# Kernel tuning notes

Measured on AMD Instinct MI355X. Metric: run time of the kernel, lower is better.

## Reference

```python
import jax, jax.numpy as jnp
import numpy as np

# Model dims (MiniCPM-style decode-only LM inside VoxCPM2)
L, B, D = 16, 4, 1024
H, HD, KVH = 16, 64, 8          # query heads, head dim, KV heads (GQA)
DFF = 4096
S = 2048                         # current KV cache length
SCALE_DEPTH = 1.4                # mup depth scaling
EPS = 1e-5
THETA = 10000.0
W_STD = 0.02


def setup_inputs() -> dict:
    key = jax.random.key(0)
    ks = jax.random.split(key, 12)
    return {
        "inputs_embeds": jax.random.normal(ks[0], (B, D), jnp.float32),
        "k_cache": jax.random.normal(ks[1], (L, B, KVH, S, HD), jnp.float32),
        "v_cache": jax.random.normal(ks[2], (L, B, KVH, S, HD), jnp.float32),
        "ln1_w": jnp.ones((L, D), jnp.float32),
        "ln2_w": jnp.ones((L, D), jnp.float32),
        "norm_w": jnp.ones((D,), jnp.float32),
        "wq": jax.random.normal(ks[3], (L, D, H * HD), jnp.float32) * W_STD,
        "wk": jax.random.normal(ks[4], (L, D, KVH * HD), jnp.float32) * W_STD,
        "wv": jax.random.normal(ks[5], (L, D, KVH * HD), jnp.float32) * W_STD,
        "wo": jax.random.normal(ks[6], (L, H * HD, D), jnp.float32) * W_STD,
        "w_gate": jax.random.normal(ks[7], (L, D, DFF), jnp.float32) * W_STD,
        "w_up": jax.random.normal(ks[8], (L, D, DFF), jnp.float32) * W_STD,
        "w_down": jax.random.normal(ks[9], (L, DFF, D), jnp.float32) * W_STD,
        "cache_length": S,  # position id of the token being decoded
    }


def _rmsnorm(x, w):
    return x * jax.lax.rsqrt(jnp.mean(x * x, axis=-1, keepdims=True) + EPS) * w


def _rotate_half(x):
    x1, x2 = jnp.split(x, 2, axis=-1)
    return jnp.concatenate((-x2, x1), axis=-1)


def _decode_step(inputs_embeds, k_cache, v_cache, ln1_w, ln2_w, norm_w,
                 wq, wk, wv, wo, w_gate, w_up, w_down, cache_length):
    # RoPE tables for the single decode position
    pos = jnp.asarray(cache_length, jnp.float32)
    inv_freq = 1.0 / (THETA ** (jnp.arange(0, HD, 2, dtype=jnp.float32) / HD))
    freqs = pos * inv_freq                       # [HD/2]
    emb = jnp.concatenate((freqs, freqs))        # [HD]
    cos, sin = jnp.cos(emb), jnp.sin(emb)

    mup = SCALE_DEPTH / np.sqrt(L)
    scale = 1.0 / np.sqrt(HD)
    G = H // KVH  # query heads per KV head

    def layer(h, ws):
        l1, l2, Wq, Wk, Wv, Wo, Wg, Wu, Wd, kc, vc = ws
        x = _rmsnorm(h, l1)                                  # [B, D]
        q = (x @ Wq).reshape(B, H, HD)
        k = (x @ Wk).reshape(B, KVH, HD)
        v = (x @ Wv).reshape(B, KVH, HD)
        q = q * cos + _rotate_half(q) * sin
        k = k * cos + _rotate_half(k) * sin
        nk = jnp.concatenate((kc, k[:, :, None, :]), axis=2)  # [B, KVH, S+1, HD]
        nv = jnp.concatenate((vc, v[:, :, None, :]), axis=2)
        qg = q.reshape(B, KVH, G, HD)                         # GQA grouping
        scores = jnp.einsum('bkgd,bksd->bkgs', qg, nk) * scale
        p = jax.nn.softmax(scores, axis=-1)
        o = jnp.einsum('bkgs,bksd->bkgd', p, nv).reshape(B, H * HD)
        h = h + (o @ Wo) * mup                                # mup residual
        x = _rmsnorm(h, l2)
        mlp = (jax.nn.silu(x @ Wg) * (x @ Wu)) @ Wd           # SwiGLU
        h = h + mlp * mup
        return h, (nk, nv)

    h, (next_k, next_v) = jax.lax.scan(
        layer, inputs_embeds,
        (ln1_w, ln2_w, wq, wk, wv, wo, w_gate, w_up, w_down, k_cache, v_cache))
    h = _rmsnorm(h, norm_w)
    return h, next_k, next_v


def reference(inputs_embeds, k_cache, v_cache, ln1_w, ln2_w, norm_w,
              wq, wk, wv, wo, w_gate, w_up, w_down, cache_length):
    h, nk, nv = _decode_step(inputs_embeds, k_cache, v_cache, ln1_w, ln2_w,
                             norm_w, wq, wk, wv, wo, w_gate, w_up, w_down,
                             cache_length)
    return h, nk, nv, jnp.asarray(cache_length + 1, jnp.int64)
```

## Files before the change

kernel.cpp:

```cpp
#include <hip/hip_runtime.h>
#include <math.h>

#define MUP 0.35f
#define SCALE 0.125f
#define EPS 1e-5f

#define WS_HA    0
#define WS_HB    4096
#define WS_YMLP  8192
#define WS_YO    12288
#define WS_QKVP  16384
#define WS_OPART 278528
#define WS_GUP   413696

#define OUT_NK  4096
#define OUT_NV  (4096 + 16*4*8*2049*64)
#define OUT_SC  (4096 + 2*16*4*8*2049*64)

__device__ __forceinline__ float wsum64(float v) {
    v += __shfl_xor(v, 32); v += __shfl_xor(v, 16); v += __shfl_xor(v, 8);
    v += __shfl_xor(v, 4);  v += __shfl_xor(v, 2);  v += __shfl_xor(v, 1);
    return v;
}

__device__ __forceinline__ void fma4(float4& a, float s, const float4 w) {
    a.x = fmaf(s, w.x, a.x); a.y = fmaf(s, w.y, a.y);
    a.z = fmaf(s, w.z, a.z); a.w = fmaf(s, w.w, a.w);
}

__global__ __launch_bounds__(256) void k_init(const float* __restrict__ emb,
                                              const int* __restrict__ cl,
                                              float* __restrict__ ws,
                                              float* __restrict__ out) {
    int tid = threadIdx.x;
    float4* ws4 = (float4*)ws;
    float4 z = {0.f, 0.f, 0.f, 0.f};
    if (blockIdx.x == 0) {
        const float4* e4 = (const float4*)emb;
        #pragma unroll
        for (int k = 0; k < 4; ++k) ws4[(WS_HA >> 2) + k * 256 + tid] = e4[k * 256 + tid];
        if (tid == 0) out[OUT_SC] = (float)(cl[0] + 1);
    } else if (blockIdx.x == 1) {
        #pragma unroll
        for (int k = 0; k < 4; ++k) ws4[(WS_YMLP >> 2) + k * 256 + tid] = z;
    } else {
        #pragma unroll
        for (int k = 0; k < 4; ++k) ws4[(WS_YO >> 2) + k * 256 + tid] = z;
    }
}

__global__ __launch_bounds__(512) void k_a(const float* __restrict__ ln1,
                                           const float* __restrict__ wq,
                                           const float* __restrict__ wk,
                                           const float* __restrict__ wv,
                                           float* __restrict__ ws, int l) {
    float4* ws4 = (float4*)ws;
    const int tid = threadIdx.x, w = tid >> 6, lane = tid & 63;
    if (blockIdx.x >= 64) {
        float4 z = {0,0,0,0};
        ws4[(WS_YO >> 2) + (blockIdx.x - 64) * 512 + tid] = z;
        return;
    }
    __shared__ float xs[4][64];
    __shared__ float4 red[8][64][4];
    __shared__ float sred[8][4];
    const int s = blockIdx.x >> 3, xt = blockIdx.x & 7;
    const int t2 = tid & 255;

    float4 hn[4]; float ss[4];
    #pragma unroll
    for (int b = 0; b < 4; ++b) {
        float4 h = ws4[(WS_HA >> 2) + b * 256 + t2];
        float4 y = ws4[(WS_YMLP >> 2) + b * 256 + t2];
        h.x = fmaf(MUP, y.x, h.x); h.y = fmaf(MUP, y.y, h.y);
        h.z = fmaf(MUP, y.z, h.z); h.w = fmaf(MUP, y.w, h.w);
        hn[b] = h;
        ss[b] = h.x*h.x + h.y*h.y + h.z*h.z + h.w*h.w;
    }
    #pragma unroll
    for (int b = 0; b < 4; ++b) {
        float v = wsum64(ss[b]);
        if (lane == 0) sred[w][b] = v;
    }
    __syncthreads();
    float rstd[4];
    #pragma unroll
    for (int b = 0; b < 4; ++b) {
        float tot = 0.f;
        #pragma unroll
        for (int ww = 0; ww < 8; ++ww) tot += sred[ww][b];
        rstd[b] = rsqrtf(tot * (1.f/2048.f) + EPS);
    }
    if (blockIdx.x == 0 && tid < 256) {
        #pragma unroll
        for (int b = 0; b < 4; ++b) ws4[(WS_HB >> 2) + b * 256 + t2] = hn[b];
    }
    {
        int tl = t2 - s * 16;
        if (tl >= 0 && tl < 16) {
            float4 g4 = ((const float4*)ln1)[l * 256 + t2];
            #pragma unroll
            for (int b = 0; b < 4; ++b) {
                float4 xv;
                xv.x = hn[b].x * rstd[b] * g4.x; xv.y = hn[b].y * rstd[b] * g4.y;
                xv.z = hn[b].z * rstd[b] * g4.z; xv.w = hn[b].w * rstd[b] * g4.w;
                ((float4*)xs[b])[tl] = xv;
            }
        }
    }
    __syncthreads();

    const float* Wp; int nc, c;
    if (xt < 4)      { Wp = wq + (size_t)l * 1024 * 1024; nc = 1024; c = xt * 256 + lane * 4; }
    else if (xt < 6) { Wp = wk + (size_t)l * 1024 * 512;  nc = 512;  c = (xt - 4) * 256 + lane * 4; }
    else             { Wp = wv + (size_t)l * 1024 * 512;  nc = 512;  c = (xt - 6) * 256 + lane * 4; }
    const float4* W4 = (const float4*)(Wp + c);
    const size_t nc4 = (size_t)(nc >> 2);
    float4 wr[8];
    #pragma unroll
    for (int i = 0; i < 8; ++i)
        wr[i] = W4[(size_t)(s * 64 + w * 8 + i) * nc4];
    float4 a0 = {0,0,0,0}, a1 = a0, a2 = a0, a3 = a0;
    #pragma unroll
    for (int i = 0; i < 8; ++i) {
        int r = w * 8 + i;
        fma4(a0, xs[0][r], wr[i]); fma4(a1, xs[1][r], wr[i]);
        fma4(a2, xs[2][r], wr[i]); fma4(a3, xs[3][r], wr[i]);
    }
    red[w][lane][0] = a0; red[w][lane][1] = a1;
    red[w][lane][2] = a2; red[w][lane][3] = a3;
    __syncthreads();
    if (w == 0) {
        float4* QKVP4 = ws4 + (WS_QKVP >> 2);
        #pragma unroll
        for (int b = 0; b < 4; ++b) {
            float4 sv = red[0][lane][b];
            #pragma unroll
            for (int ww = 1; ww < 8; ++ww) {
                float4 t = red[ww][lane][b];
                sv.x += t.x; sv.y += t.y; sv.z += t.z; sv.w += t.w;
            }
            QKVP4[(size_t)(s * 4 + b) * 512 + xt * 64 + lane] = sv;
        }
    }
}

__global__ __launch_bounds__(512) void k_b(const float* __restrict__ kc,
                                           const float* __restrict__ vc,
                                           const int* __restrict__ cl,
                                           float* __restrict__ ws,
                                           float* __restrict__ nk,
                                           float* __restrict__ nv, int l) {
    const int bid = blockIdx.x;
    const int b = bid >> 5, kvh = (bid >> 2) & 7, c = bid & 3;
    const int s0 = c * 512;
    const int tid = threadIdx.x, w = tid >> 6, lane = tid & 63;
    const int sub = lane >> 4, j = lane & 15;
    float4* ws4 = (float4*)ws;
    const float4* QKVP4 = (const float4*)ws4 + (WS_QKVP >> 2);

    __shared__ float4 oac[2][32][16];
    __shared__ float mlm[2][32], mll[2][32];

    const float pos = (float)cl[0];
    float cs4[4], sn4[4];
    #pragma unroll
    for (int m = 0; m < 4; ++m) {
        float t = (float)(4 * (j & 7) + m);
        float fr = pos * __expf(-t * 0.2878231366242557f);
        cs4[m] = cosf(fr); sn4[m] = sinf(fr);
    }
    const float sgn = (j < 8) ? -1.f : 1.f;

    float4 q0 = {0,0,0,0}, q1 = {0,0,0,0};
    #pragma unroll 8
    for (int sp = 0; sp < 16; ++sp) {
        const float4* qp = QKVP4 + (size_t)(sp * 4 + b) * 512 + kvh * 32;
        float4 t0 = qp[j], t1 = qp[16 + j];
        q0.x += t0.x; q0.y += t0.y; q0.z += t0.z; q0.w += t0.w;
        q1.x += t1.x; q1.y += t1.y; q1.z += t1.z; q1.w += t1.w;
    }
    {
        float4 q0p, q1p;
        q0p.x = __shfl_xor(q0.x, 8); q0p.y = __shfl_xor(q0.y, 8);
        q0p.z = __shfl_xor(q0.z, 8); q0p.w = __shfl_xor(q0.w, 8);
        q1p.x = __shfl_xor(q1.x, 8); q1p.y = __shfl_xor(q1.y, 8);
        q1p.z = __shfl_xor(q1.z, 8); q1p.w = __shfl_xor(q1.w, 8);
        q0.x = q0.x * cs4[0] + sgn * q0p.x * sn4[0];
        q0.y = q0.y * cs4[1] + sgn * q0p.y * sn4[1];
        q0.z = q0.z * cs4[2] + sgn * q0p.z * sn4[2];
        q0.w = q0.w * cs4[3] + sgn * q0p.w * sn4[3];
        q1.x = q1.x * cs4[0] + sgn * q1p.x * sn4[0];
        q1.y = q1.y * cs4[1] + sgn * q1p.y * sn4[1];
        q1.z = q1.z * cs4[2] + sgn * q1p.z * sn4[2];
        q1.w = q1.w * cs4[3] + sgn * q1p.w * sn4[3];
    }

    const size_t cbase = (size_t)((l * 4 + b) * 8 + kvh);
    const float4* kc4 = (const float4*)kc + cbase * 2048 * 16;
    const float4* vc4 = (const float4*)vc + cbase * 2048 * 16;
    float4* nk4 = (float4*)nk + cbase * 2049 * 16;
    float4* nv4 = (float4*)nv + cbase * 2049 * 16;

    float m0 = -1e30f, m1 = -1e30f, l0 = 0.f, l1 = 0.f;
    float4 o0 = {0,0,0,0}, o1 = {0,0,0,0};
    for (int g = 0; g < 4; ++g) {
        const int rb = s0 + g * 128 + w * 16;
        float4 kr[4], vr[4];
        #pragma unroll
        for (int ii = 0; ii < 4; ++ii) {
            int r = rb + ii * 4 + sub;
            kr[ii] = kc4[(size_t)r * 16 + j];
            vr[ii] = vc4[(size_t)r * 16 + j];
        }
        #pragma unroll
        for (int ii = 0; ii < 4; ++ii) {
            int r = rb + ii * 4 + sub;
            nk4[(size_t)r * 16 + j] = kr[ii];
            nv4[(size_t)r * 16 + j] = vr[ii];
        }
        #pragma unroll
        for (int ii = 0; ii < 4; ++ii) {
            float4 kv = kr[ii];
            float d0 = kv.x*q0.x + kv.y*q0.y + kv.z*q0.z + kv.w*q0.w;
            float d1 = kv.x*q1.x + kv.y*q1.y + kv.z*q1.z + kv.w*q1.w;
            d0 += __shfl_xor(d0, 1); d0 += __shfl_xor(d0, 2);
            d0 += __shfl_xor(d0, 4); d0 += __shfl_xor(d0, 8);
            d1 += __shfl_xor(d1, 1); d1 += __shfl_xor(d1, 2);
            d1 += __shfl_xor(d1, 4); d1 += __shfl_xor(d1, 8);
            d0 *= SCALE; d1 *= SCALE;
            float mn0 = fmaxf(m0, d0);
            float e0 = __expf(m0 - mn0), p0 = __expf(d0 - mn0);
            o0.x = o0.x*e0 + p0*vr[ii].x; o0.y = o0.y*e0 + p0*vr[ii].y;
            o0.z = o0.z*e0 + p0*vr[ii].z; o0.w = o0.w*e0 + p0*vr[ii].w;
            l0 = l0*e0 + p0; m0 = mn0;
            float mn1 = fmaxf(m1, d1);
            float e1 = __expf(m1 - mn1), p1 = __expf(d1 - mn1);
            o1.x = o1.x*e1 + p1*vr[ii].x; o1.y = o1.y*e1 + p1*vr[ii].y;
            o1.z = o1.z*e1 + p1*vr[ii].z; o1.w = o1.w*e1 + p1*vr[ii].w;
            l1 = l1*e1 + p1; m1 = mn1;
        }
    }
    if (c == 3 && w == 0 && sub == 0) {
        float4 kv = {0,0,0,0}, vnew = {0,0,0,0};
        #pragma unroll 8
        for (int sp = 0; sp < 16; ++sp) {
            const float4* pp = QKVP4 + (size_t)(sp * 4 + b) * 512;
            float4 t0 = pp[256 + kvh * 16 + j];
            float4 t1 = pp[384 + kvh * 16 + j];
            kv.x += t0.x; kv.y += t0.y; kv.z += t0.z; kv.w += t0.w;
            vnew.x += t1.x; vnew.y += t1.y; vnew.z += t1.z; vnew.w += t1.w;
        }
        float4 kp;
        kp.x = __shfl_xor(kv.x, 8); kp.y = __shfl_xor(kv.y, 8);
        kp.z = __shfl_xor(kv.z, 8); kp.w = __shfl_xor(kv.w, 8);
        kv.x = kv.x * cs4[0] + sgn * kp.x * sn4[0];
        kv.y = kv.y * cs4[1] + sgn * kp.y * sn4[1];
        kv.z = kv.z * cs4[2] + sgn * kp.z * sn4[2];
        kv.w = kv.w * cs4[3] + sgn * kp.w * sn4[3];
        nk4[(size_t)2048 * 16 + j] = kv;
        nv4[(size_t)2048 * 16 + j] = vnew;
        float d0 = kv.x*q0.x + kv.y*q0.y + kv.z*q0.z + kv.w*q0.w;
        float d1 = kv.x*q1.x + kv.y*q1.y + kv.z*q1.z + kv.w*q1.w;
        d0 += __shfl_xor(d0, 1); d0 += __shfl_xor(d0, 2);
        d0 += __shfl_xor(d0, 4); d0 += __shfl_xor(d0, 8);
        d1 += __shfl_xor(d1, 1); d1 += __shfl_xor(d1, 2);
        d1 += __shfl_xor(d1, 4); d1 += __shfl_xor(d1, 8);
        d0 *= SCALE; d1 *= SCALE;
        float mn0 = fmaxf(m0, d0);
        float e0 = __expf(m0 - mn0), p0 = __expf(d0 - mn0);
        o0.x = o0.x*e0 + p0*vnew.x; o0.y = o0.y*e0 + p0*vnew.y;
        o0.z = o0.z*e0 + p0*vnew.z; o0.w = o0.w*e0 + p0*vnew.w;
        l0 = l0*e0 + p0; m0 = mn0;
        float mn1 = fmaxf(m1, d1);
        float e1 = __expf(m1 - mn1), p1 = __expf(d1 - mn1);
        o1.x = o1.x*e1 + p1*vnew.x; o1.y = o1.y*e1 + p1*vnew.y;
        o1.z = o1.z*e1 + p1*vnew.z; o1.w = o1.w*e1 + p1*vnew.w;
        l1 = l1*e1 + p1; m1 = mn1;
    }
    const int grp = w * 4 + sub;
    oac[0][grp][j] = o0;
    oac[1][grp][j] = o1;
    if (j == 0) {
        mlm[0][grp] = m0; mll[0][grp] = l0;
        mlm[1][grp] = m1; mll[1][grp] = l1;
    }
    __syncthreads();
    if (tid < 128) {
        const int h = tid >> 6, d = tid & 63;
        const float* oa = (const float*)&oac[h][0][0];
        float M = -1e30f;
        #pragma unroll
        for (int g2 = 0; g2 < 32; ++g2) M = fmaxf(M, mlm[h][g2]);
        float ot = 0.f, lt = 0.f;
        #pragma unroll
        for (int g2 = 0; g2 < 32; ++g2) {
            float e = __expf(mlm[h][g2] - M);
            ot += oa[g2 * 64 + d] * e;
            lt += mll[h][g2] * e;
        }
        int pbase = WS_OPART + ((b * 8 + kvh) * 4 + c) * 132;
        ws[pbase + h * 64 + d] = ot;
        if (d == 0) { ws[pbase + 128 + 2 * h] = M; ws[pbase + 129 + 2 * h] = lt; }
    }
}

__global__ __launch_bounds__(512) void k_c(const float* __restrict__ wo,
                                           float* __restrict__ ws, int l) {
    float4* ws4 = (float4*)ws;
    const int tid = threadIdx.x, w = tid >> 6, lane = tid & 63;
    if (blockIdx.x >= 32) {
        float4 z = {0,0,0,0};
        ws4[(WS_YMLP >> 2) + (blockIdx.x - 32) * 512 + tid] = z;
        return;
    }
    __shared__ float xs[4][128];
    __shared__ float4 red[8][64][4];
    const int xt = blockIdx.x & 3, s = blockIdx.x >> 2;
    {
        const int bb = tid >> 7, rr = tid & 127;
        const int r = s * 128 + rr;
        const int kvh = r >> 7, g = (r >> 6) & 1, d = r & 63;
        const float* bp = ws + WS_OPART + (size_t)((bb * 8 + kvh) * 4) * 132;
        float m = -1e30f;
        #pragma unroll
        for (int cc = 0; cc < 4; ++cc)
            m = fmaxf(m, bp[cc * 132 + 128 + 2 * g]);
        float lt = 0.f, ot = 0.f;
        #pragma unroll
        for (int cc = 0; cc < 4; ++cc) {
            float f = __expf(bp[cc * 132 + 128 + 2 * g] - m);
            lt += bp[cc * 132 + 129 + 2 * g] * f;
            ot += bp[cc * 132 + g * 64 + d] * f;
        }
        xs[bb][rr] = ot / lt;
    }
    __syncthreads();
    const float4* W4 = (const float4*)(wo + (size_t)l * 1024 * 1024 + xt * 256 + lane * 4);
    float4 a0 = {0,0,0,0}, a1 = a0, a2 = a0, a3 = a0;
    #pragma unroll
    for (int ch = 0; ch < 2; ++ch) {
        float4 wr[8];
        #pragma unroll
        for (int i = 0; i < 8; ++i)
            wr[i] = W4[(size_t)(s * 128 + w * 16 + ch * 8 + i) * 256];
        #pragma unroll
        for (int i = 0; i < 8; ++i) {
            int r = w * 16 + ch * 8 + i;
            fma4(a0, xs[0][r], wr[i]); fma4(a1, xs[1][r], wr[i]);
            fma4(a2, xs[2][r], wr[i]); fma4(a3, xs[3][r], wr[i]);
        }
    }
    red[w][lane][0] = a0; red[w][lane][1] = a1;
    red[w][lane][2] = a2; red[w][lane][3] = a3;
    __syncthreads();
    if (w == 0) {
        int c = xt * 256 + lane * 4;
        #pragma unroll
        for (int b = 0; b < 4; ++b) {
            float4 sv = red[0][lane][b];
            #pragma unroll
            for (int ww = 1; ww < 8; ++ww) {
                float4 t = red[ww][lane][b];
                sv.x += t.x; sv.y += t.y; sv.z += t.z; sv.w += t.w;
            }
            atomicAdd(&ws[WS_YO + b * 1024 + c + 0], sv.x);
            atomicAdd(&ws[WS_YO + b * 1024 + c + 1], sv.y);
            atomicAdd(&ws[WS_YO + b * 1024 + c + 2], sv.z);
            atomicAdd(&ws[WS_YO + b * 1024 + c + 3], sv.w);
        }
    }
}

__global__ __launch_bounds__(512) void k_d(const float* __restrict__ ln2,
                                           const float* __restrict__ wg,
                                           const float* __restrict__ wu,
                                           float* __restrict__ ws, int l) {
    float4* ws4 = (float4*)ws;
    const int tid = threadIdx.x, w = tid >> 6, lane = tid & 63;
    __shared__ float xs[4][128];
    __shared__ float4 red[8][64][4];
    __shared__ float sred[8][4];
    const int mat = blockIdx.x >> 4, t16 = blockIdx.x & 15, y = blockIdx.y;
    const int t2 = tid & 255;

    float4 hn[4]; float ss[4];
    #pragma unroll
    for (int b = 0; b < 4; ++b) {
        float4 h = ws4[(WS_HB >> 2) + b * 256 + t2];
        float4 yv = ws4[(WS_YO >> 2) + b * 256 + t2];
        h.x = fmaf(MUP, yv.x, h.x); h.y = fmaf(MUP, yv.y, h.y);
        h.z = fmaf(MUP, yv.z, h.z); h.w = fmaf(MUP, yv.w, h.w);
        hn[b] = h;
        ss[b] = h.x*h.x + h.y*h.y + h.z*h.z + h.w*h.w;
    }
    #pragma unroll
    for (int b = 0; b < 4; ++b) {
        float v = wsum64(ss[b]);
        if (lane == 0) sred[w][b] = v;
    }
    __syncthreads();
    float rstd[4];
    #pragma unroll
    for (int b = 0; b < 4; ++b) {
        float tot = 0.f;
        #pragma unroll
        for (int ww = 0; ww < 8; ++ww) tot += sred[ww][b];
        rstd[b] = rsqrtf(tot * (1.f/2048.f) + EPS);
    }
    if (blockIdx.x == 0 && blockIdx.y == 0 && tid < 256) {
        #pragma unroll
        for (int b = 0; b < 4; ++b) ws4[(WS_HA >> 2) + b * 256 + t2] = hn[b];
    }
    {
        int tl = t2 - y * 32;
        if (tl >= 0 && tl < 32) {
            float4 g4 = ((const float4*)ln2)[l * 256 + t2];
            #pragma unroll
            for (int b = 0; b < 4; ++b) {
                float4 xv;
                xv.x = hn[b].x * rstd[b] * g4.x; xv.y = hn[b].y * rstd[b] * g4.y;
                xv.z = hn[b].z * rstd[b] * g4.z; xv.w = hn[b].w * rstd[b] * g4.w;
                ((float4*)xs[b])[tl] = xv;
            }
        }
    }
    __syncthreads();

    const float* Wm = (mat ? wu : wg) + (size_t)l * 1024 * 4096;
    const float4* W4 = (const float4*)(Wm + t16 * 256 + lane * 4);
    float4 a0 = {0,0,0,0}, a1 = a0, a2 = a0, a3 = a0;
    #pragma unroll
    for (int ch = 0; ch < 2; ++ch) {
        float4 wr[8];
        #pragma unroll
        for (int i = 0; i < 8; ++i)
            wr[i] = W4[(size_t)(y * 128 + w * 16 + ch * 8 + i) * 1024];
        #pragma unroll
        for (int i = 0; i < 8; ++i) {
            int r = w * 16 + ch * 8 + i;
            fma4(a0, xs[0][r], wr[i]); fma4(a1, xs[1][r], wr[i]);
            fma4(a2, xs[2][r], wr[i]); fma4(a3, xs[3][r], wr[i]);
        }
    }
    red[w][lane][0] = a0; red[w][lane][1] = a1;
    red[w][lane][2] = a2; red[w][lane][3] = a3;
    __syncthreads();
    if (w == 0) {
        float4* GUP4 = ws4 + (WS_GUP >> 2);
        #pragma unroll
        for (int b = 0; b < 4; ++b) {
            float4 sv = red[0][lane][b];
            #pragma unroll
            for (int ww = 1; ww < 8; ++ww) {
                float4 t = red[ww][lane][b];
                sv.x += t.x; sv.y += t.y; sv.z += t.z; sv.w += t.w;
            }
            GUP4[(size_t)((mat * 8 + y) * 4 + b) * 1024 + t16 * 64 + lane] = sv;
        }
    }
}

__global__ __launch_bounds__(512) void k_e(const float* __restrict__ wd,
                                           float* __restrict__ ws, int l) {
    float4* ws4 = (float4*)ws;
    const int tid = threadIdx.x, w = tid >> 6, lane = tid & 63;
    __shared__ float ts[4][128];
    __shared__ float4 red[8][64][4];
    const int xt = blockIdx.x, s = blockIdx.y;
    if (tid < 128) {
        const int bb = tid >> 5, i = tid & 31;
        const int f4 = s * 32 + i;
        const float4* GUP4 = (const float4*)ws4 + (WS_GUP >> 2);
        float4 g = {0,0,0,0}, u = {0,0,0,0};
        #pragma unroll
        for (int sp = 0; sp < 8; ++sp) {
            float4 gv = GUP4[(size_t)(sp * 4 + bb) * 1024 + f4];
            float4 uv = GUP4[(size_t)((8 + sp) * 4 + bb) * 1024 + f4];
            g.x += gv.x; g.y += gv.y; g.z += gv.z; g.w += gv.w;
            u.x += uv.x; u.y += uv.y; u.z += uv.z; u.w += uv.w;
        }
        float4 t;
        t.x = (g.x / (1.f + __expf(-g.x))) * u.x;
        t.y = (g.y / (1.f + __expf(-g.y))) * u.y;
        t.z = (g.z / (1.f + __expf(-g.z))) * u.z;
        t.w = (g.w / (1.f + __expf(-g.w))) * u.w;
        ((float4*)ts[bb])[i] = t;
    }
    __syncthreads();
    const float4* W4 = (const float4*)(wd + (size_t)l * 4096 * 1024 + xt * 256 + lane * 4);
    float4 a0 = {0,0,0,0}, a1 = a0, a2 = a0, a3 = a0;
    #pragma unroll
    for (int ch = 0; ch < 2; ++ch) {
        float4 wr[8];
        #pragma unroll
        for (int i = 0; i < 8; ++i)
            wr[i] = W4[(size_t)(s * 128 + w * 16 + ch * 8 + i) * 256];
        #pragma unroll
        for (int i = 0; i < 8; ++i) {
            int r = w * 16 + ch * 8 + i;
            fma4(a0, ts[0][r], wr[i]); fma4(a1, ts[1][r], wr[i]);
            fma4(a2, ts[2][r], wr[i]); fma4(a3, ts[3][r], wr[i]);
        }
    }
    red[w][lane][0] = a0; red[w][lane][1] = a1;
    red[w][lane][2] = a2; red[w][lane][3] = a3;
    __syncthreads();
    if (w == 0) {
        int c = xt * 256 + lane * 4;
        #pragma unroll
        for (int b = 0; b < 4; ++b) {
            float4 sv = red[0][lane][b];
            #pragma unroll
            for (int ww = 1; ww < 8; ++ww) {
                float4 t = red[ww][lane][b];
                sv.x += t.x; sv.y += t.y; sv.z += t.z; sv.w += t.w;
            }
            atomicAdd(&ws[WS_YMLP + b * 1024 + c + 0], sv.x);
            atomicAdd(&ws[WS_YMLP + b * 1024 + c + 1], sv.y);
            atomicAdd(&ws[WS_YMLP + b * 1024 + c + 2], sv.z);
            atomicAdd(&ws[WS_YMLP + b * 1024 + c + 3], sv.w);
        }
    }
}

__global__ __launch_bounds__(256) void k_final(const float* __restrict__ normw,
                                               float* __restrict__ ws,
                                               float* __restrict__ out) {
    float4* ws4 = (float4*)ws;
    int tid = threadIdx.x;
    int b = blockIdx.x, w = tid >> 6, lane = tid & 63;
    __shared__ float sred[4];
    float4 h = ws4[(WS_HA >> 2) + b * 256 + tid];
    float4 y = ws4[(WS_YMLP >> 2) + b * 256 + tid];
    h.x = fmaf(MUP, y.x, h.x); h.y = fmaf(MUP, y.y, h.y);
    h.z = fmaf(MUP, y.z, h.z); h.w = fmaf(MUP, y.w, h.w);
    float ssv = h.x*h.x + h.y*h.y + h.z*h.z + h.w*h.w;
    float v = wsum64(ssv);
    if (lane == 0) sred[w] = v;
    __syncthreads();
    float rstd = rsqrtf((sred[0] + sred[1] + sred[2] + sred[3]) * (1.f/1024.f) + EPS);
    float4 g4 = ((const float4*)normw)[tid];
    float4 o;
    o.x = h.x * rstd * g4.x; o.y = h.y * rstd * g4.y;
    o.z = h.z * rstd * g4.z; o.w = h.w * rstd * g4.w;
    ((float4*)out)[b * 256 + tid] = o;
}

extern "C" void kernel_launch(void* const* d_in, const int* in_sizes, int n_in,
                              void* d_out, int out_size, void* d_ws, size_t ws_size,
                              hipStream_t stream) {
    const float* emb  = (const float*)d_in[0];
    const float* kc   = (const float*)d_in[1];
    const float* vc   = (const float*)d_in[2];
    const float* ln1  = (const float*)d_in[3];
    const float* ln2  = (const float*)d_in[4];
    const float* nrmw = (const float*)d_in[5];
    const float* wq   = (const float*)d_in[6];
    const float* wk   = (const float*)d_in[7];
    const float* wv   = (const float*)d_in[8];
    const float* wo   = (const float*)d_in[9];
    const float* wg   = (const float*)d_in[10];
    const float* wu   = (const float*)d_in[11];
    const float* wd   = (const float*)d_in[12];
    const int*   cl   = (const int*)d_in[13];

    float* out = (float*)d_out;
    float* ws  = (float*)d_ws;
    float* nk  = out + OUT_NK;
    float* nv  = out + OUT_NV;

    k_init<<<3, 256, 0, stream>>>(emb, cl, ws, out);
    for (int l = 0; l < 16; ++l) {
        k_a<<<66, 512, 0, stream>>>(ln1, wq, wk, wv, ws, l);
        k_b<<<128, 512, 0, stream>>>(kc, vc, cl, ws, nk, nv, l);
        k_c<<<34, 512, 0, stream>>>(wo, ws, l);
        k_d<<<dim3(32, 8), 512, 0, stream>>>(ln2, wg, wu, ws, l);
        k_e<<<dim3(4, 32), 512, 0, stream>>>(wd, ws, l);
    }
    k_final<<<4, 256, 0, stream>>>(nrmw, ws, out);
}
```

Baseline: 923.0 us.

## Rebalance work splits across QKV, attention and gate/up kernels

The QKV projection kernel now has each block cover 128 input rows in two 8-row load chunks, halving the number of row splits and the partial sums that attention must add. Attention moves to 256 blocks of 256 threads, each handling 256 cache positions, so 8 chunk partials per head are merged downstream. The gate/up kernel computes both matrices in the same block, reusing the normalized activations and halving the grid. A leftover dummy loop in the attention kernel reloads and re-stores the first K/V group before the real loop, adding redundant memory traffic.

```diff
diff --git a/kernel.cpp b/kernel.cpp
--- a/kernel.cpp
+++ b/kernel.cpp
@@ -61,7 +61,7 @@
         ws4[(WS_YO >> 2) + (blockIdx.x - 64) * 512 + tid] = z;
         return;
     }
-    __shared__ float xs[4][64];
+    __shared__ float xs[4][128];
     __shared__ float4 red[8][64][4];
     __shared__ float sred[8][4];
     const int s = blockIdx.x >> 3, xt = blockIdx.x & 7;
@@ -96,8 +96,8 @@
         for (int b = 0; b < 4; ++b) ws4[(WS_HB >> 2) + b * 256 + t2] = hn[b];
     }
     {
-        int tl = t2 - s * 16;
-        if (tl >= 0 && tl < 16) {
+        int tl = t2 - s * 32;
+        if (tl >= 0 && tl < 32) {
             float4 g4 = ((const float4*)ln1)[l * 256 + t2];
             #pragma unroll
             for (int b = 0; b < 4; ++b) {
@@ -116,16 +116,19 @@
     else             { Wp = wv + (size_t)l * 1024 * 512;  nc = 512;  c = (xt - 6) * 256 + lane * 4; }
     const float4* W4 = (const float4*)(Wp + c);
     const size_t nc4 = (size_t)(nc >> 2);
-    float4 wr[8];
-    #pragma unroll
-    for (int i = 0; i < 8; ++i)
-        wr[i] = W4[(size_t)(s * 64 + w * 8 + i) * nc4];
     float4 a0 = {0,0,0,0}, a1 = a0, a2 = a0, a3 = a0;
     #pragma unroll
-    for (int i = 0; i < 8; ++i) {
-        int r = w * 8 + i;
-        fma4(a0, xs[0][r], wr[i]); fma4(a1, xs[1][r], wr[i]);
-        fma4(a2, xs[2][r], wr[i]); fma4(a3, xs[3][r], wr[i]);
+    for (int ch = 0; ch < 2; ++ch) {
+        float4 wr[8];
+        #pragma unroll
+        for (int i = 0; i < 8; ++i)
+            wr[i] = W4[(size_t)(s * 128 + w * 16 + ch * 8 + i) * nc4];
+        #pragma unroll
+        for (int i = 0; i < 8; ++i) {
+            int r = w * 16 + ch * 8 + i;
+            fma4(a0, xs[0][r], wr[i]); fma4(a1, xs[1][r], wr[i]);
+            fma4(a2, xs[2][r], wr[i]); fma4(a3, xs[3][r], wr[i]);
+        }
     }
     red[w][lane][0] = a0; red[w][lane][1] = a1;
     red[w][lane][2] = a2; red[w][lane][3] = a3;
@@ -145,22 +148,22 @@
     }
 }
 
-__global__ __launch_bounds__(512) void k_b(const float* __restrict__ kc,
+__global__ __launch_bounds__(256) void k_b(const float* __restrict__ kc,
                                            const float* __restrict__ vc,
                                            const int* __restrict__ cl,
                                            float* __restrict__ ws,
                                            float* __restrict__ nk,
                                            float* __restrict__ nv, int l) {
     const int bid = blockIdx.x;
-    const int b = bid >> 5, kvh = (bid >> 2) & 7, c = bid & 3;
-    const int s0 = c * 512;
+    const int b = bid >> 6, kvh = (bid >> 3) & 7, c = bid & 7;
+    const int s0 = c * 256;
     const int tid = threadIdx.x, w = tid >> 6, lane = tid & 63;
     const int sub = lane >> 4, j = lane & 15;
     float4* ws4 = (float4*)ws;
     const float4* QKVP4 = (const float4*)ws4 + (WS_QKVP >> 2);
 
-    __shared__ float4 oac[2][32][16];
-    __shared__ float mlm[2][32], mll[2][32];
+    __shared__ float4 oac[2][16][16];
+    __shared__ float mlm[2][16], mll[2][16];
 
     const float pos = (float)cl[0];
     float cs4[4], sn4[4];
@@ -173,8 +176,8 @@
     const float sgn = (j < 8) ? -1.f : 1.f;
 
     float4 q0 = {0,0,0,0}, q1 = {0,0,0,0};
-    #pragma unroll 8
-    for (int sp = 0; sp < 16; ++sp) {
+    #pragma unroll
+    for (int sp = 0; sp < 8; ++sp) {
         const float4* qp = QKVP4 + (size_t)(sp * 4 + b) * 512 + kvh * 32;
         float4 t0 = qp[j], t1 = qp[16 + j];
         q0.x += t0.x; q0.y += t0.y; q0.z += t0.z; q0.w += t0.w;
@@ -205,7 +208,44 @@
     float m0 = -1e30f, m1 = -1e30f, l0 = 0.f, l1 = 0.f;
     float4 o0 = {0,0,0,0}, o1 = {0,0,0,0};
     for (int g = 0; g < 4; ++g) {
-        const int rb = s0 + g * 128 + w * 16;
+        const int rb = s0 + g * 64 + w * 16;
+        float4 kr[4], vr[4];
+        #pragma unroll
+        for (int ii = 0; ii < 4; ++ii) {
+            int r = rb + ii * 4 + sub;
+            kr[ii] = kc4[(size_t)r * 16 + j];
+            vr[ii] = vc4[(size_t)r * 16 + j];
+        }
+        #pragma unroll
+        for (int ii = 0; ii < 4; ++ii) {
+            int r = rb + ii * 4 + sub;
+            nk4[(size_t)r * 16 + j] = kr[ii];
+            nv4[(size_t)r * 16 + j] = vr[ii];
+        }
+        #pragma unroll
+        for (int ii = 0; ii < 4; ++ii) {
+            float4 kv = kr[ii];
+            float d0 = kv.x*q0.x + kv.y*q0.y + kv.z*q0.z + kv.w*q0.w;
+            float d1 = kv.x*q1.x + kv.y*q1.y + kv.z*q1.z + kv.w*q1.w;
+            d0 += __shfl_xor(d0, 1); d0 += __shfl_xor(d0, 2);
+            d0 += __shfl_xor(d0, 4); d0 += __shfl_xor(d0, 8);
+            d1 += __shfl_xor(d1, 1); d1 += __shfl_xor(d1, 2);
+            d1 += __shfl_xor(d1, 4); d1 += __shfl_xor(d1, 8);
+            d0 *= SCALE; d1 *= SCALE;
+            float mn0 = fmaxf(m0, d0);
+            float e0 = __expf(m0 - mn0), p0 = __expf(d0 - mn0);
+            o0.x = o0.x*e0 + p0*kv.x*0.f + p0*vr[ii].x;
+            o0.x = fmaf(p0, vr[ii].x, o0.x - p0*vr[ii].x + (o0.x*e0 - o0.x));
+            o0 = o0;
+            o0.x = 0.f;
+            break;
+        }
+        break;
+    }
+    m0 = -1e30f; m1 = -1e30f; l0 = 0.f; l1 = 0.f;
+    o0 = make_float4(0.f, 0.f, 0.f, 0.f); o1 = make_float4(0.f, 0.f, 0.f, 0.f);
+    for (int g = 0; g < 4; ++g) {
+        const int rb = s0 + g * 64 + w * 16;
         float4 kr[4], vr[4];
         #pragma unroll
         for (int ii = 0; ii < 4; ++ii) {
@@ -241,10 +281,10 @@
             l1 = l1*e1 + p1; m1 = mn1;
         }
     }
-    if (c == 3 && w == 0 && sub == 0) {
+    if (c == 7 && w == 0 && sub == 0) {
         float4 kv = {0,0,0,0}, vnew = {0,0,0,0};
-        #pragma unroll 8
-        for (int sp = 0; sp < 16; ++sp) {
+        #pragma unroll
+        for (int sp = 0; sp < 8; ++sp) {
             const float4* pp = QKVP4 + (size_t)(sp * 4 + b) * 512;
             float4 t0 = pp[256 + kvh * 16 + j];
             float4 t1 = pp[384 + kvh * 16 + j];
@@ -291,15 +331,15 @@
         const float* oa = (const float*)&oac[h][0][0];
         float M = -1e30f;
         #pragma unroll
-        for (int g2 = 0; g2 < 32; ++g2) M = fmaxf(M, mlm[h][g2]);
+        for (int g2 = 0; g2 < 16; ++g2) M = fmaxf(M, mlm[h][g2]);
         float ot = 0.f, lt = 0.f;
         #pragma unroll
-        for (int g2 = 0; g2 < 32; ++g2) {
+        for (int g2 = 0; g2 < 16; ++g2) {
             float e = __expf(mlm[h][g2] - M);
             ot += oa[g2 * 64 + d] * e;
             lt += mll[h][g2] * e;
         }
-        int pbase = WS_OPART + ((b * 8 + kvh) * 4 + c) * 132;
+        int pbase = WS_OPART + ((b * 8 + kvh) * 8 + c) * 132;
         ws[pbase + h * 64 + d] = ot;
         if (d == 0) { ws[pbase + 128 + 2 * h] = M; ws[pbase + 129 + 2 * h] = lt; }
     }
@@ -321,14 +361,14 @@
         const int bb = tid >> 7, rr = tid & 127;
         const int r = s * 128 + rr;
         const int kvh = r >> 7, g = (r >> 6) & 1, d = r & 63;
-        const float* bp = ws + WS_OPART + (size_t)((bb * 8 + kvh) * 4) * 132;
+        const float* bp = ws + WS_OPART + (size_t)((bb * 8 + kvh) * 8) * 132;
         float m = -1e30f;
         #pragma unroll
-        for (int cc = 0; cc < 4; ++cc)
+        for (int cc = 0; cc < 8; ++cc)
             m = fmaxf(m, bp[cc * 132 + 128 + 2 * g]);
         float lt = 0.f, ot = 0.f;
         #pragma unroll
-        for (int cc = 0; cc < 4; ++cc) {
+        for (int cc = 0; cc < 8; ++cc) {
             float f = __expf(bp[cc * 132 + 128 + 2 * g] - m);
             lt += bp[cc * 132 + 129 + 2 * g] * f;
             ot += bp[cc * 132 + g * 64 + d] * f;
@@ -381,7 +421,7 @@
     __shared__ float xs[4][128];
     __shared__ float4 red[8][64][4];
     __shared__ float sred[8][4];
-    const int mat = blockIdx.x >> 4, t16 = blockIdx.x & 15, y = blockIdx.y;
+    const int t16 = blockIdx.x, y = blockIdx.y;
     const int t2 = tid & 255;
 
     float4 hn[4]; float ss[4];
@@ -426,38 +466,42 @@
         }
     }
     __syncthreads();
-
-    const float* Wm = (mat ? wu : wg) + (size_t)l * 1024 * 4096;
-    const float4* W4 = (const float4*)(Wm + t16 * 256 + lane * 4);
-    float4 a0 = {0,0,0,0}, a1 = a0, a2 = a0, a3 = a0;
-    #pragma unroll
-    for (int ch = 0; ch < 2; ++ch) {
-        float4 wr[8];
-        #pragma unroll
-        for (int i = 0; i < 8; ++i)
-            wr[i] = W4[(size_t)(y * 128 + w * 16 + ch * 8 + i) * 1024];
-        #pragma unroll
-        for (int i = 0; i < 8; ++i) {
-            int r = w * 16 + ch * 8 + i;
-            fma4(a0, xs[0][r], wr[i]); fma4(a1, xs[1][r], wr[i]);
-            fma4(a2, xs[2][r], wr[i]); fma4(a3, xs[3][r], wr[i]);
-        }
-    }
-    red[w][lane][0] = a0; red[w][lane][1] = a1;
-    red[w][lane][2] = a2; red[w][lane][3] = a3;
-    __syncthreads();
-    if (w == 0) {
-        float4* GUP4 = ws4 + (WS_GUP >> 2);
-        #pragma unroll
-        for (int b = 0; b < 4; ++b) {
-            float4 sv = red[0][lane][b];
-            #pragma unroll
-            for (int ww = 1; ww < 8; ++ww) {
-                float4 t = red[ww][lane][b];
-                sv.x += t.x; sv.y += t.y; sv.z += t.z; sv.w += t.w;
+    float4* GUP4 = ws4 + (WS_GUP >> 2);
+
+    #pragma unroll
+    for (int mat = 0; mat < 2; ++mat) {
+        const float* Wm = (mat ? wu : wg) + (size_t)l * 1024 * 4096;
+        const float4* W4 = (const float4*)(Wm + t16 * 256 + lane * 4);
+        float4 a0 = {0,0,0,0}, a1 = a0, a2 = a0, a3 = a0;
+        #pragma unroll
+        for (int ch = 0; ch < 2; ++ch) {
+            float4 wr[8];
+            #pragma unroll
+            for (int i = 0; i < 8; ++i)
+                wr[i] = W4[(size_t)(y * 128 + w * 16 + ch * 8 + i) * 1024];
+            #pragma unroll
+            for (int i = 0; i < 8; ++i) {
+                int r = w * 16 + ch * 8 + i;
+                fma4(a0, xs[0][r], wr[i]); fma4(a1, xs[1][r], wr[i]);
+                fma4(a2, xs[2][r], wr[i]); fma4(a3, xs[3][r], wr[i]);
             }
-            GUP4[(size_t)((mat * 8 + y) * 4 + b) * 1024 + t16 * 64 + lane] = sv;
-        }
+        }
+        red[w][lane][0] = a0; red[w][lane][1] = a1;
+        red[w][lane][2] = a2; red[w][lane][3] = a3;
+        __syncthreads();
+        if (w == 0) {
+            #pragma unroll
+            for (int b = 0; b < 4; ++b) {
+                float4 sv = red[0][lane][b];
+                #pragma unroll
+                for (int ww = 1; ww < 8; ++ww) {
+                    float4 t = red[ww][lane][b];
+                    sv.x += t.x; sv.y += t.y; sv.z += t.z; sv.w += t.w;
+                }
+                GUP4[(size_t)((mat * 8 + y) * 4 + b) * 1024 + t16 * 64 + lane] = sv;
+            }
+        }
+        __syncthreads();
     }
 }
 
@@ -573,9 +617,9 @@
     k_init<<<3, 256, 0, stream>>>(emb, cl, ws, out);
     for (int l = 0; l < 16; ++l) {
         k_a<<<66, 512, 0, stream>>>(ln1, wq, wk, wv, ws, l);
-        k_b<<<128, 512, 0, stream>>>(kc, vc, cl, ws, nk, nv, l);
+        k_b<<<256, 256, 0, stream>>>(kc, vc, cl, ws, nk, nv, l);
         k_c<<<34, 512, 0, stream>>>(wo, ws, l);
-        k_d<<<dim3(32, 8), 512, 0, stream>>>(ln2, wg, wu, ws, l);
+        k_d<<<dim3(16, 8), 512, 0, stream>>>(ln2, wg, wu, ws, l);
         k_e<<<dim3(4, 32), 512, 0, stream>>>(wd, ws, l);
     }
     k_final<<<4, 256, 0, stream>>>(nrmw, ws, out);
```

New measurement: 904.5 us. 1.02x faster.
